# Optimization experiments

Hardware: AMD Instinct MI355X
Metric: run time of the kernel (lower is better)

The kernel has to match this reference:

```python
import jax, jax.numpy as jnp
import numpy as np

NUM_HEADS = 8
HEAD_CH = 32  # embed_channels // num_heads = 256 // 8
BN_EPS = 1e-3


def _conv(x, w, pad):
    return jax.lax.conv_general_dilated(
        x, w, window_strides=(1, 1), padding=[(pad, pad), (pad, pad)],
        dimension_numbers=('NCHW', 'OIHW', 'NCHW'))


def _bn(x, gamma, beta):
    # inference BN with running_mean=0, running_var=1 (fresh buffers)
    scale = gamma / jnp.sqrt(1.0 + BN_EPS)
    return x * scale[None, :, None, None] + beta[None, :, None, None]


def setup_inputs() -> dict:
    key = jax.random.key(0)
    ks = jax.random.split(key, 8)
    B, Cin, H, W = 16, 512, 40, 40
    N, Cg, E, Cout = 80, 512, 256, 512
    s = 0.05
    return {
        'x': jax.random.normal(ks[0], (B, Cin, H, W), jnp.float32),
        'guide': jax.random.normal(ks[1], (B, N, Cg), jnp.float32),
        'We': jax.random.normal(ks[2], (E, Cin, 1, 1), jnp.float32) * s,
        'gamma_e': jnp.ones((E,), jnp.float32),
        'beta_e': jnp.zeros((E,), jnp.float32),
        'Wg': jax.random.normal(ks[3], (E, Cg), jnp.float32) * s,
        'bg': jnp.zeros((E,), jnp.float32),
        'head_bias': jnp.zeros((NUM_HEADS,), jnp.float32),
        'Wp': jax.random.normal(ks[4], (Cout, Cin, 3, 3), jnp.float32) * s,
        'gamma_p': jnp.ones((Cout,), jnp.float32),
        'beta_p': jnp.zeros((Cout,), jnp.float32),
    }


def reference(x, guide, We, gamma_e, beta_e, Wg, bg, head_bias, Wp, gamma_p, beta_p):
    B, _, H, W = x.shape
    M, C = NUM_HEADS, HEAD_CH
    # guide_fc: [B, n, Cg] -> [B, n, M, C]
    g = (jnp.einsum('bnc,ec->bne', guide, Wg) + bg).reshape(B, -1, M, C)
    # embed_conv (1x1 + BN, no act): [B, M, C, H, W]
    e = _bn(_conv(x, We, 0), gamma_e, beta_e).reshape(B, M, C, H, W)
    # attention scores, max over guide tokens, scale, bias, sigmoid
    attn = jnp.einsum('bmchw,bnmc->bmhwn', e, g)
    attn = jnp.max(attn, axis=-1) / (C ** 0.5)
    attn = jax.nn.sigmoid(attn + head_bias[None, :, None, None])
    # project_conv (3x3 + BN, no act), gated per head
    p = _bn(_conv(x, Wp, 1), gamma_p, beta_p)
    p = p.reshape(B, M, -1, H, W) * attn[:, :, None, :, :]
    return p.reshape(B, -1, H, W)
```

## Files before the change

### kernel.cpp

```cpp
#include <hip/hip_runtime.h>
#include <hip/hip_bf16.h>
#include <stdint.h>

#define B_   16
#define CIN  512
#define HW   1600
#define E_   256
#define NTOK 80
#define CG   512
#define COUT 512
#define NHEAD 8
#define HCH  32
#define SP   (42*42)

typedef __attribute__((ext_vector_type(8))) short bf16x8;
typedef __attribute__((ext_vector_type(4))) float f32x4;

__device__ __forceinline__ unsigned short f2bf(float f) {
  union { float f; unsigned int i; } v; v.f = f;
  unsigned int x = v.i;
  return (unsigned short)((x + 0x7FFFu + ((x >> 16) & 1u)) >> 16);
}

__global__ void k_prep_x(const float* __restrict__ x, unsigned short* __restrict__ xt) {
  __shared__ float tile[32][33];
  int hw0 = blockIdx.x * 32, ci0 = blockIdx.y * 32, b = blockIdx.z;
  int tx = threadIdx.x, ty = threadIdx.y;
  const float* xp = x + ((size_t)b * CIN + ci0) * HW + hw0;
#pragma unroll
  for (int j = 0; j < 4; j++) tile[ty + 8 * j][tx] = xp[(size_t)(ty + 8 * j) * HW + tx];
  __syncthreads();
  int ci = ci0 + tx;
#pragma unroll
  for (int j = 0; j < 4; j++) {
    int hw = hw0 + ty + 8 * j;
    int h = hw / 40, w = hw - h * 40;
    xt[((size_t)b * SP + (size_t)(h + 1) * 42 + (w + 1)) * CIN + ci] = f2bf(tile[tx][ty + 8 * j]);
  }
}

__global__ void k_prep_wp(const float* __restrict__ Wp, unsigned short* __restrict__ wpb2) {
  int idx = blockIdx.x * 256 + threadIdx.x;
  int co = idx >> 9, ci = idx & 511;
  const float* s = Wp + (size_t)idx * 9;
#pragma unroll
  for (int t = 0; t < 9; t++) wpb2[(size_t)co * (9 * CIN) + t * CIN + ci] = f2bf(s[t]);
}

__global__ void k_cast_all(const float* __restrict__ We, unsigned short* __restrict__ web,
                           const float* __restrict__ Wg, unsigned short* __restrict__ wgb,
                           const float* __restrict__ gu, unsigned short* __restrict__ gub) {
  int i = blockIdx.x * 256 + threadIdx.x;
  const float* src; unsigned short* dst; int j;
  if (i < 32768)       { src = We; dst = web; j = i; }
  else if (i < 65536)  { src = Wg; dst = wgb; j = i - 32768; }
  else                 { src = gu; dst = gub; j = i - 65536; }
  float4 v = ((const float4*)src)[j];
  ushort4 o; o.x = f2bf(v.x); o.y = f2bf(v.y); o.z = f2bf(v.z); o.w = f2bf(v.w);
  ((ushort4*)dst)[j] = o;
}

template<int NTAPS, int EPI, int MT, int NT, int SWZ>
__launch_bounds__(256, 2)
__global__ void k_conv(const unsigned short* __restrict__ Aw,
                       const unsigned short* __restrict__ Bsrc,
                       const float* __restrict__ gamma, const float* __restrict__ beta,
                       const float* __restrict__ attn, float* __restrict__ outp,
                       unsigned short* __restrict__ et) {
  constexpr int  RS    = NTAPS * CIN;
  constexpr int  NSTEP = NTAPS * (CIN / 32);
  constexpr bool BLIN  = (EPI == 2);
  __shared__ unsigned short L[3 * 12288];
  char* LB = (char*)L;
  int tid = threadIdx.x;

  int wg = blockIdx.x;
  if constexpr (SWZ) {
    constexpr int q = MT * NT / 8;
    wg = (wg & 7) * q + (wg >> 3);
  }
  int mtile = wg / NT, ntile = wg % NT;
  int m0 = mtile * 256, n0 = ntile * 128;

  int lane = tid & 63, wid = tid >> 6;
  int wr = wid >> 1, wc = wid & 1;

  int rA = tid >> 2;
  int kq = ((tid & 3) ^ ((tid >> 3) & 3)) * 8;
  const unsigned short* pA = Aw + (size_t)(m0 + rA) * RS + kq;
  const unsigned short* pB0;
  const unsigned short* pB1;
  if constexpr (BLIN) {
    pB0 = Bsrc + (size_t)(n0 + rA) * CIN + kq;
    pB1 = pB0 + (size_t)64 * CIN;
  } else {
    int c0 = n0 + rA, c1 = c0 + 64;
    int b0 = c0 / 1600, hw0 = c0 - b0 * 1600;
    int b1 = c1 / 1600, hw1 = c1 - b1 * 1600;
    int h0 = hw0 / 40, w0 = hw0 - h0 * 40;
    int h1 = hw1 / 40, w1 = hw1 - h1 * 40;
    constexpr int ctr = (NTAPS == 1) ? 43 : 0;
    pB0 = Bsrc + ((size_t)b0 * SP + h0 * 42 + w0 + ctr) * CIN + kq;
    pB1 = Bsrc + ((size_t)b1 * SP + h1 * 42 + w1 + ctr) * CIN + kq;
  }

  int scnt = 0;
  auto STG = [&](unsigned bo) {
#define GL(src, dst) __builtin_amdgcn_global_load_lds((const __attribute__((address_space(1))) unsigned int*)(src), \
        (__attribute__((address_space(3))) unsigned int*)(dst), 16, 0, 0)
    GL(pA,            LB + bo +      0u + tid * 16u);
    GL(pA +  64 * RS, LB + bo +  4096u + tid * 16u);
    GL(pA + 128 * RS, LB + bo +  8192u + tid * 16u);
    GL(pA + 192 * RS, LB + bo + 12288u + tid * 16u);
    GL(pB0,           LB + bo + 16384u + tid * 16u);
    GL(pB1,           LB + bo + 20480u + tid * 16u);
#undef GL
    pA += 32; pB0 += 32; pB1 += 32;
    if constexpr (NTAPS > 1) {
      ++scnt;
      if ((scnt % 48) == 0) { pB0 += 19968; pB1 += 19968; }
    }
  };

  int frow = lane & 15;
  int swz = ((lane >> 4) ^ ((frow >> 1) & 3)) << 4;
  int aoff[8], boff[4];
#pragma unroll
  for (int i = 0; i < 8; i++) aoff[i] = (wr * 128 + i * 16 + frow) * 64 + swz;
#pragma unroll
  for (int i = 0; i < 4; i++) boff[i] = 16384 + (wc * 64 + i * 16 + frow) * 64 + swz;

  f32x4 acc[8][4] = {};

  STG(0u); STG(24576u);
  unsigned r0 = 0u, r1 = 24576u, r2 = 49152u;
  for (int s = 0; s < NSTEP; ++s) {
    if (s + 1 < NSTEP) { asm volatile("s_waitcnt vmcnt(6)" ::: "memory"); }
    else               { asm volatile("s_waitcnt vmcnt(0)" ::: "memory"); }
    __builtin_amdgcn_s_barrier();
    __builtin_amdgcn_sched_barrier(0);
    if (s + 2 < NSTEP) STG(r2);
    const char* base = LB + r0;
    bf16x8 af[8], bv[4];
#pragma unroll
    for (int i = 0; i < 8; i++) af[i] = *(const bf16x8*)(base + aoff[i]);
#pragma unroll
    for (int i = 0; i < 4; i++) bv[i] = *(const bf16x8*)(base + boff[i]);
#pragma unroll
    for (int mi = 0; mi < 8; mi++)
#pragma unroll
      for (int ni = 0; ni < 4; ni++)
        acc[mi][ni] = __builtin_amdgcn_mfma_f32_16x16x32_bf16(af[mi], bv[ni], acc[mi][ni], 0, 0, 0);
    unsigned t = r0; r0 = r1; r1 = r2; r2 = t;
  }

  const float BN_RSQ = 0.9995003746877732f;
  int colb = n0 + wc * 64 + frow;
  int rowb = m0 + wr * 128 + (lane >> 4) * 4;
  if constexpr (EPI == 1) {
    float* ob = outp;
#pragma unroll
    for (int mi = 0; mi < 8; mi++) {
      int head = (m0 + wr * 128 + mi * 16) >> 6;
      float sc[4], bt[4];
#pragma unroll
      for (int j = 0; j < 4; j++) {
        int co = rowb + mi * 16 + j;
        sc[j] = gamma[co] * BN_RSQ; bt[j] = beta[co];
      }
#pragma unroll
      for (int ni = 0; ni < 4; ni++) {
        int col = colb + ni * 16;
        int b = col / 1600, hw = col - b * 1600;
        float gate = attn[((size_t)b * NHEAD + head) * HW + hw];
#pragma unroll
        for (int j = 0; j < 4; j++) {
          int co = rowb + mi * 16 + j;
          ob[((size_t)b * COUT + co) * HW + hw] = (acc[mi][ni][j] * sc[j] + bt[j]) * gate;
        }
      }
    }
  } else {
#pragma unroll
    for (int mi = 0; mi < 8; mi++) {
      float sc[4], bt[4];
#pragma unroll
      for (int j = 0; j < 4; j++) {
        int ech = rowb + mi * 16 + j;
        sc[j] = (EPI == 2) ? 1.0f : gamma[ech] * BN_RSQ;
        bt[j] = beta[ech];
      }
#pragma unroll
      for (int ni = 0; ni < 4; ni++) {
        int col = colb + ni * 16;
        size_t rowbase;
        if constexpr (EPI == 2) {
          rowbase = (size_t)col * E_;
        } else {
          int b = col / 1600, hw = col - b * 1600;
          rowbase = ((size_t)b * HW + hw) * E_;
        }
        ushort4 pk;
        pk.x = f2bf(acc[mi][ni][0] * sc[0] + bt[0]);
        pk.y = f2bf(acc[mi][ni][1] * sc[1] + bt[1]);
        pk.z = f2bf(acc[mi][ni][2] * sc[2] + bt[2]);
        pk.w = f2bf(acc[mi][ni][3] * sc[3] + bt[3]);
        *(ushort4*)(et + rowbase + (rowb + mi * 16)) = pk;
      }
    }
  }
}

__global__ void k_attn_mfma(const unsigned short* __restrict__ et, const unsigned short* __restrict__ gbf,
                            const float* __restrict__ head_bias, float* __restrict__ attn) {
  __shared__ unsigned short gs[NTOK * HCH];
  int b = blockIdx.z, m = blockIdx.y;
  int tid = threadIdx.x, lane = tid & 63, wid = tid >> 6;
  for (int i = tid; i < NTOK * HCH / 8; i += 256) {
    int n = i >> 2, c = (i & 3) * 8;
    *(bf16x8*)&gs[n * HCH + c] = *(const bf16x8*)&gbf[((size_t)b * NTOK + n) * E_ + m * HCH + c];
  }
  __syncthreads();
  int col = lane & 15, kq = (lane >> 4) * 8;
  bf16x8 bfr[5];
#pragma unroll
  for (int ni = 0; ni < 5; ni++)
    bfr[ni] = *(const bf16x8*)&gs[(ni * 16 + col) * HCH + kq];

  int hw0 = blockIdx.x * 256 + wid * 64;
  bf16x8 afr[4];
#pragma unroll
  for (int mi = 0; mi < 4; mi++) {
    int hw = hw0 + mi * 16 + col; if (hw > HW - 1) hw = HW - 1;
    afr[mi] = *(const bf16x8*)&et[((size_t)b * HW + hw) * E_ + m * HCH + kq];
  }
  float hb = head_bias[m];
  float* attnp = attn + ((size_t)b * NHEAD + m) * HW;
#pragma unroll
  for (int mi = 0; mi < 4; mi++) {
    f32x4 d[5];
#pragma unroll
    for (int ni = 0; ni < 5; ni++) {
      f32x4 z = {0.f, 0.f, 0.f, 0.f};
      d[ni] = __builtin_amdgcn_mfma_f32_16x16x32_bf16(afr[mi], bfr[ni], z, 0, 0, 0);
    }
#pragma unroll
    for (int j = 0; j < 4; j++) {
      float v = fmaxf(fmaxf(fmaxf(d[0][j], d[1][j]), fmaxf(d[2][j], d[3][j])), d[4][j]);
      v = fmaxf(v, __shfl_xor(v, 1, 16));
      v = fmaxf(v, __shfl_xor(v, 2, 16));
      v = fmaxf(v, __shfl_xor(v, 4, 16));
      v = fmaxf(v, __shfl_xor(v, 8, 16));
      if (col == j) {
        int hwout = hw0 + mi * 16 + (lane >> 4) * 4 + j;
        if (hwout < HW)
          attnp[hwout] = 1.0f / (1.0f + __expf(-(v * 0.17677669529663687f + hb)));
      }
    }
  }
}

extern "C" void kernel_launch(void* const* d_in, const int* in_sizes, int n_in,
                              void* d_out, int out_size, void* d_ws, size_t ws_size,
                              hipStream_t stream) {
  const float* x         = (const float*)d_in[0];
  const float* guide     = (const float*)d_in[1];
  const float* We        = (const float*)d_in[2];
  const float* gamma_e   = (const float*)d_in[3];
  const float* beta_e    = (const float*)d_in[4];
  const float* Wg        = (const float*)d_in[5];
  const float* bg        = (const float*)d_in[6];
  const float* head_bias = (const float*)d_in[7];
  const float* Wp        = (const float*)d_in[8];
  const float* gamma_p   = (const float*)d_in[9];
  const float* beta_p    = (const float*)d_in[10];
  float* out = (float*)d_out;

  char* ws = (char*)d_ws;
  size_t off = 0;
  auto alloc = [&](size_t bytes) { char* p = ws + off; off += (bytes + 255) & ~(size_t)255; return p; };
  unsigned short* xt   = (unsigned short*)alloc((size_t)B_ * SP * CIN * 2);
  unsigned short* wpb2 = (unsigned short*)alloc((size_t)COUT * 9 * CIN * 2);
  unsigned short* web  = (unsigned short*)alloc((size_t)E_ * CIN * 2);
  unsigned short* wgb  = (unsigned short*)alloc((size_t)E_ * CG * 2);
  unsigned short* gub  = (unsigned short*)alloc((size_t)B_ * NTOK * CG * 2);
  unsigned short* gbf  = (unsigned short*)alloc((size_t)B_ * NTOK * E_ * 2);
  unsigned short* et   = (unsigned short*)alloc((size_t)B_ * HW * E_ * 2);
  float* attn          = (float*)alloc((size_t)B_ * NHEAD * HW * 4);

  hipMemsetAsync(xt, 0, (size_t)B_ * SP * CIN * 2, stream);
  k_prep_x<<<dim3(50, 16, B_), dim3(32, 8), 0, stream>>>(x, xt);
  k_prep_wp<<<dim3(1024), dim3(256), 0, stream>>>(Wp, wpb2);
  k_cast_all<<<dim3(896), dim3(256), 0, stream>>>(We, web, Wg, wgb, guide, gub);
  k_conv<1, 2, 1, 10, 0><<<dim3(10), dim3(256), 0, stream>>>(wgb, gub, bg, bg, nullptr, nullptr, gbf);
  k_conv<1, 0, 1, 200, 1><<<dim3(200), dim3(256), 0, stream>>>(web, xt, gamma_e, beta_e, nullptr, nullptr, et);
  k_attn_mfma<<<dim3(7, NHEAD, B_), dim3(256), 0, stream>>>(et, gbf, head_bias, attn);
  k_conv<9, 1, 2, 200, 1><<<dim3(400), dim3(256), 0, stream>>>(wpb2, xt, gamma_p, beta_p, attn, out, nullptr);
}
```

Baseline: 309.5 us.

## Fuse all three GEMMs into one launch with 256x256 tiles and separate gate pass

```diff
diff --git a/kernel.cpp b/kernel.cpp
--- a/kernel.cpp
+++ b/kernel.cpp
@@ -60,152 +60,179 @@
   ((ushort4*)dst)[j] = o;
 }
 
-template<int NTAPS, int EPI, int MT, int NT, int SWZ>
-__launch_bounds__(256, 2)
-__global__ void k_conv(const unsigned short* __restrict__ Aw,
-                       const unsigned short* __restrict__ Bsrc,
-                       const float* __restrict__ gamma, const float* __restrict__ beta,
-                       const float* __restrict__ attn, float* __restrict__ outp,
-                       unsigned short* __restrict__ et) {
-  constexpr int  RS    = NTAPS * CIN;
-  constexpr int  NSTEP = NTAPS * (CIN / 32);
-  constexpr bool BLIN  = (EPI == 2);
-  __shared__ unsigned short L[3 * 12288];
+__global__ __launch_bounds__(512, 2)
+void k_fused(const unsigned short* __restrict__ wpb2, const unsigned short* __restrict__ web,
+             const unsigned short* __restrict__ wgb,  const unsigned short* __restrict__ xt,
+             const unsigned short* __restrict__ gub,
+             const float* __restrict__ gamma_e, const float* __restrict__ beta_e,
+             const float* __restrict__ gamma_p, const float* __restrict__ beta_p,
+             const float* __restrict__ bg,
+             float* __restrict__ out, unsigned short* __restrict__ et,
+             unsigned short* __restrict__ gbf) {
+  __shared__ unsigned short L[3 * 16384];
   char* LB = (char*)L;
   int tid = threadIdx.x;
-
   int wg = blockIdx.x;
-  if constexpr (SWZ) {
-    constexpr int q = MT * NT / 8;
-    wg = (wg & 7) * q + (wg >> 3);
-  }
-  int mtile = wg / NT, ntile = wg % NT;
-  int m0 = mtile * 256, n0 = ntile * 128;
+
+  int role, m0, n0;
+  if (wg < 200)      { int w = (wg & 7) * 25 + (wg >> 3);
+                       role = 0; m0 = (w / 100) * 256; n0 = (w % 100) * 256; }
+  else if (wg < 300) { role = 1; m0 = 0; n0 = (wg - 200) * 256; }
+  else               { role = 2; m0 = 0; n0 = (wg - 300) * 256; }
+
+  const int RS    = (role == 0) ? 9 * CIN : CIN;
+  const int NSTEP = (role == 0) ? 144 : 16;
+  const bool tapjump = (role == 0);
+  const unsigned short* Aw = (role == 0) ? wpb2 : (role == 1) ? web : wgb;
 
   int lane = tid & 63, wid = tid >> 6;
-  int wr = wid >> 1, wc = wid & 1;
-
-  int rA = tid >> 2;
-  int kq = ((tid & 3) ^ ((tid >> 3) & 3)) * 8;
-  const unsigned short* pA = Aw + (size_t)(m0 + rA) * RS + kq;
+  int wr = wid >> 2, wc = wid & 3;
+
+  int rloc = tid >> 2;
+  int kq_g = ((tid & 3) ^ ((tid >> 3) & 3)) * 8;
+  const unsigned short* pA = Aw + (size_t)(m0 + rloc) * RS + kq_g;
   const unsigned short* pB0;
   const unsigned short* pB1;
-  if constexpr (BLIN) {
-    pB0 = Bsrc + (size_t)(n0 + rA) * CIN + kq;
-    pB1 = pB0 + (size_t)64 * CIN;
+  if (role == 2) {
+    pB0 = gub + (size_t)(n0 + rloc) * CIN + kq_g;
+    pB1 = pB0 + (size_t)128 * CIN;
   } else {
-    int c0 = n0 + rA, c1 = c0 + 64;
+    int c0 = n0 + rloc, c1 = c0 + 128;
     int b0 = c0 / 1600, hw0 = c0 - b0 * 1600;
     int b1 = c1 / 1600, hw1 = c1 - b1 * 1600;
     int h0 = hw0 / 40, w0 = hw0 - h0 * 40;
     int h1 = hw1 / 40, w1 = hw1 - h1 * 40;
-    constexpr int ctr = (NTAPS == 1) ? 43 : 0;
-    pB0 = Bsrc + ((size_t)b0 * SP + h0 * 42 + w0 + ctr) * CIN + kq;
-    pB1 = Bsrc + ((size_t)b1 * SP + h1 * 42 + w1 + ctr) * CIN + kq;
+    int ctr = (role == 1) ? 43 : 0;
+    pB0 = xt + ((size_t)b0 * SP + h0 * 42 + w0 + ctr) * CIN + kq_g;
+    pB1 = xt + ((size_t)b1 * SP + h1 * 42 + w1 + ctr) * CIN + kq_g;
   }
 
   int scnt = 0;
-  auto STG = [&](unsigned bo) {
 #define GL(src, dst) __builtin_amdgcn_global_load_lds((const __attribute__((address_space(1))) unsigned int*)(src), \
         (__attribute__((address_space(3))) unsigned int*)(dst), 16, 0, 0)
-    GL(pA,            LB + bo +      0u + tid * 16u);
-    GL(pA +  64 * RS, LB + bo +  4096u + tid * 16u);
+  auto STG_A = [&](unsigned bo) {
+    GL(pA,            LB + bo +     0u + tid * 16u);
     GL(pA + 128 * RS, LB + bo +  8192u + tid * 16u);
-    GL(pA + 192 * RS, LB + bo + 12288u + tid * 16u);
+  };
+  auto STG_B = [&](unsigned bo) {
     GL(pB0,           LB + bo + 16384u + tid * 16u);
-    GL(pB1,           LB + bo + 20480u + tid * 16u);
-#undef GL
+    GL(pB1,           LB + bo + 24576u + tid * 16u);
+  };
+  auto ADV = [&]() {
     pA += 32; pB0 += 32; pB1 += 32;
-    if constexpr (NTAPS > 1) {
-      ++scnt;
-      if ((scnt % 48) == 0) { pB0 += 19968; pB1 += 19968; }
-    }
+    if (tapjump) { ++scnt; if ((scnt % 48) == 0) { pB0 += 19968; pB1 += 19968; } }
   };
 
   int frow = lane & 15;
-  int swz = ((lane >> 4) ^ ((frow >> 1) & 3)) << 4;
+  int sg = ((lane >> 4) ^ ((frow >> 1) & 3)) << 4;
   int aoff[8], boff[4];
 #pragma unroll
-  for (int i = 0; i < 8; i++) aoff[i] = (wr * 128 + i * 16 + frow) * 64 + swz;
-#pragma unroll
-  for (int i = 0; i < 4; i++) boff[i] = 16384 + (wc * 64 + i * 16 + frow) * 64 + swz;
+  for (int i = 0; i < 8; i++) aoff[i] = (wr * 128 + i * 16 + frow) * 64 + sg;
+#pragma unroll
+  for (int i = 0; i < 4; i++) boff[i] = 16384 + (wc * 64 + i * 16 + frow) * 64 + sg;
 
   f32x4 acc[8][4] = {};
 
-  STG(0u); STG(24576u);
-  unsigned r0 = 0u, r1 = 24576u, r2 = 49152u;
+  STG_A(0u); STG_B(0u); ADV();
+  STG_A(32768u); STG_B(32768u); ADV();
+  unsigned r0 = 0u, r1 = 32768u, r2 = 65536u;
+
   for (int s = 0; s < NSTEP; ++s) {
-    if (s + 1 < NSTEP) { asm volatile("s_waitcnt vmcnt(6)" ::: "memory"); }
+    if (s + 1 < NSTEP) { asm volatile("s_waitcnt vmcnt(4)" ::: "memory"); }
     else               { asm volatile("s_waitcnt vmcnt(0)" ::: "memory"); }
     __builtin_amdgcn_s_barrier();
     __builtin_amdgcn_sched_barrier(0);
-    if (s + 2 < NSTEP) STG(r2);
     const char* base = LB + r0;
+    bool pre = (s + 2 < NSTEP);
     bf16x8 af[8], bv[4];
 #pragma unroll
-    for (int i = 0; i < 8; i++) af[i] = *(const bf16x8*)(base + aoff[i]);
+    for (int i = 0; i < 4; i++) af[i] = *(const bf16x8*)(base + aoff[i]);
 #pragma unroll
     for (int i = 0; i < 4; i++) bv[i] = *(const bf16x8*)(base + boff[i]);
-#pragma unroll
-    for (int mi = 0; mi < 8; mi++)
+    if (pre) STG_A(r2);
+    __builtin_amdgcn_s_barrier();
+    __builtin_amdgcn_s_setprio(1);
+#pragma unroll
+    for (int mi = 0; mi < 4; mi++)
 #pragma unroll
       for (int ni = 0; ni < 4; ni++)
         acc[mi][ni] = __builtin_amdgcn_mfma_f32_16x16x32_bf16(af[mi], bv[ni], acc[mi][ni], 0, 0, 0);
+    __builtin_amdgcn_s_setprio(0);
+    __builtin_amdgcn_s_barrier();
+#pragma unroll
+    for (int i = 4; i < 8; i++) af[i] = *(const bf16x8*)(base + aoff[i]);
+    if (pre) { STG_B(r2); ADV(); }
+    __builtin_amdgcn_s_barrier();
+    __builtin_amdgcn_s_setprio(1);
+#pragma unroll
+    for (int mi = 4; mi < 8; mi++)
+#pragma unroll
+      for (int ni = 0; ni < 4; ni++)
+        acc[mi][ni] = __builtin_amdgcn_mfma_f32_16x16x32_bf16(af[mi], bv[ni], acc[mi][ni], 0, 0, 0);
+    __builtin_amdgcn_s_setprio(0);
     unsigned t = r0; r0 = r1; r1 = r2; r2 = t;
   }
+#undef GL
 
   const float BN_RSQ = 0.9995003746877732f;
   int colb = n0 + wc * 64 + frow;
   int rowb = m0 + wr * 128 + (lane >> 4) * 4;
-  if constexpr (EPI == 1) {
-    float* ob = outp;
+  if (role == 0) {
 #pragma unroll
     for (int mi = 0; mi < 8; mi++) {
-      int head = (m0 + wr * 128 + mi * 16) >> 6;
       float sc[4], bt[4];
 #pragma unroll
       for (int j = 0; j < 4; j++) {
         int co = rowb + mi * 16 + j;
-        sc[j] = gamma[co] * BN_RSQ; bt[j] = beta[co];
+        sc[j] = gamma_p[co] * BN_RSQ; bt[j] = beta_p[co];
       }
 #pragma unroll
       for (int ni = 0; ni < 4; ni++) {
         int col = colb + ni * 16;
         int b = col / 1600, hw = col - b * 1600;
-        float gate = attn[((size_t)b * NHEAD + head) * HW + hw];
 #pragma unroll
         for (int j = 0; j < 4; j++) {
           int co = rowb + mi * 16 + j;
-          ob[((size_t)b * COUT + co) * HW + hw] = (acc[mi][ni][j] * sc[j] + bt[j]) * gate;
+          out[((size_t)b * COUT + co) * HW + hw] = acc[mi][ni][j] * sc[j] + bt[j];
         }
       }
     }
-  } else {
+  } else if (role == 1) {
 #pragma unroll
     for (int mi = 0; mi < 8; mi++) {
       float sc[4], bt[4];
 #pragma unroll
       for (int j = 0; j < 4; j++) {
         int ech = rowb + mi * 16 + j;
-        sc[j] = (EPI == 2) ? 1.0f : gamma[ech] * BN_RSQ;
-        bt[j] = beta[ech];
+        sc[j] = gamma_e[ech] * BN_RSQ; bt[j] = beta_e[ech];
       }
 #pragma unroll
       for (int ni = 0; ni < 4; ni++) {
         int col = colb + ni * 16;
-        size_t rowbase;
-        if constexpr (EPI == 2) {
-          rowbase = (size_t)col * E_;
-        } else {
-          int b = col / 1600, hw = col - b * 1600;
-          rowbase = ((size_t)b * HW + hw) * E_;
-        }
+        int b = col / 1600, hw = col - b * 1600;
         ushort4 pk;
         pk.x = f2bf(acc[mi][ni][0] * sc[0] + bt[0]);
         pk.y = f2bf(acc[mi][ni][1] * sc[1] + bt[1]);
         pk.z = f2bf(acc[mi][ni][2] * sc[2] + bt[2]);
         pk.w = f2bf(acc[mi][ni][3] * sc[3] + bt[3]);
-        *(ushort4*)(et + rowbase + (rowb + mi * 16)) = pk;
+        *(ushort4*)(et + ((size_t)b * HW + hw) * E_ + (rowb + mi * 16)) = pk;
+      }
+    }
+  } else {
+#pragma unroll
+    for (int mi = 0; mi < 8; mi++) {
+      float bt[4];
+#pragma unroll
+      for (int j = 0; j < 4; j++) bt[j] = bg[rowb + mi * 16 + j];
+#pragma unroll
+      for (int ni = 0; ni < 4; ni++) {
+        int col = colb + ni * 16;
+        ushort4 pk;
+        pk.x = f2bf(acc[mi][ni][0] + bt[0]);
+        pk.y = f2bf(acc[mi][ni][1] + bt[1]);
+        pk.z = f2bf(acc[mi][ni][2] + bt[2]);
+        pk.w = f2bf(acc[mi][ni][3] + bt[3]);
+        *(ushort4*)(gbf + (size_t)col * E_ + (rowb + mi * 16)) = pk;
       }
     }
   }
@@ -258,6 +285,18 @@
       }
     }
   }
+}
+
+__global__ void k_gate(float* __restrict__ out, const float* __restrict__ attn) {
+  int idx = blockIdx.x * 256 + threadIdx.x;
+  int f4 = idx * 4;
+  int b = f4 / (COUT * HW);
+  int rem = f4 - b * (COUT * HW);
+  int co = rem / HW, hw = rem - co * HW;
+  float4 a = *(const float4*)(attn + ((size_t)b * NHEAD + (co >> 6)) * HW + hw);
+  float4 p = ((float4*)out)[idx];
+  p.x *= a.x; p.y *= a.y; p.z *= a.z; p.w *= a.w;
+  ((float4*)out)[idx] = p;
 }
 
 extern "C" void kernel_launch(void* const* d_in, const int* in_sizes, int n_in,
@@ -292,8 +331,8 @@
   k_prep_x<<<dim3(50, 16, B_), dim3(32, 8), 0, stream>>>(x, xt);
   k_prep_wp<<<dim3(1024), dim3(256), 0, stream>>>(Wp, wpb2);
   k_cast_all<<<dim3(896), dim3(256), 0, stream>>>(We, web, Wg, wgb, guide, gub);
-  k_conv<1, 2, 1, 10, 0><<<dim3(10), dim3(256), 0, stream>>>(wgb, gub, bg, bg, nullptr, nullptr, gbf);
-  k_conv<1, 0, 1, 200, 1><<<dim3(200), dim3(256), 0, stream>>>(web, xt, gamma_e, beta_e, nullptr, nullptr, et);
+  k_fused<<<dim3(305), dim3(512), 0, stream>>>(wpb2, web, wgb, xt, gub,
+      gamma_e, beta_e, gamma_p, beta_p, bg, out, et, gbf);
   k_attn_mfma<<<dim3(7, NHEAD, B_), dim3(256), 0, stream>>>(et, gbf, head_bias, attn);
-  k_conv<9, 1, 2, 200, 1><<<dim3(400), dim3(256), 0, stream>>>(wpb2, xt, gamma_p, beta_p, attn, out, nullptr);
-}
+  k_gate<<<dim3(12800), dim3(256), 0, stream>>>(out, attn);
+}
```

Measured after the change: 302.1 us. 1.02x faster.
